# Kernel optimization log

Hardware: AMD Instinct MI355X
Metric: run time of the kernel (lower is better)

## Reference

```python
import jax, jax.numpy as jnp
import numpy as np

EPS = 1e-12  # torch F.normalize eps


def setup_inputs() -> dict:
    key = jax.random.key(0)
    k1, k2, k3, k4, k5 = jax.random.split(key, 5)
    N, C, H, W = 32, 512, 32, 32
    E = 1024   # expansion * dim
    G = 8      # group
    D = E // G # 128, per-group channel dim
    K = 64     # num_clusters
    x = jax.random.normal(k1, (N, C, H, W), dtype=jnp.float32)
    W1 = jax.random.normal(k2, (E, C), dtype=jnp.float32) / np.sqrt(C)
    W2 = jax.random.normal(k3, (G, E), dtype=jnp.float32) / np.sqrt(E)
    Wc = jax.random.normal(k4, (K, D), dtype=jnp.float32) / np.sqrt(D)
    centroids = jax.random.uniform(k5, (K, D), dtype=jnp.float32)
    return {"x": x, "W1": W1, "W2": W2, "Wc": Wc, "centroids": centroids}


def reference(x, W1, W2, Wc, centroids):
    # x: [N, C, H, W]; W1: [E, C]; W2: [G, E]; Wc: [K, D]; centroids: [K, D]
    N, C, H, W = x.shape
    E = W1.shape[0]
    G = W2.shape[0]
    K, D = Wc.shape
    P = H * W
    # descriptor-wise L2 normalization over channel dim
    norm = jnp.linalg.norm(x, axis=1, keepdims=True)
    x = x / jnp.maximum(norm, EPS)
    # linear1 on channels: [N, E, P]
    xe = jnp.einsum('ncp,ec->nep', x.reshape(N, C, P), W1)
    # grouped features: [N, G, D, P]
    xg = xe.reshape(N, G, D, P)
    # attention gate: sigmoid(linear2)  -> [N, G, P]
    att = jax.nn.sigmoid(jnp.einsum('nep,ge->ngp', xe, W2))
    # 1x1 conv = per-pixel matmul with cluster weights -> [N, G, K, P]
    soft_assign = jax.nn.softmax(jnp.einsum('ngdp,kd->ngkp', xg, Wc), axis=2)
    # combined per-(cluster,pixel) weight
    w = soft_assign * att[:, :, None, :]  # [N, G, K, P]
    # NetVLAD residual aggregation, algebraically decomposed to avoid the
    # giant [N,G,K,D,P] intermediate:
    #   vlad[n,k,d] = sum_{g,p} w * xg  -  centroids[k,d] * sum_{g,p} w
    agg = jnp.einsum('ngkp,ngdp->nkd', w, xg)  # [N, K, D]
    wsum = w.sum(axis=(1, 3))                  # [N, K]
    vlad = agg - wsum[:, :, None] * centroids[None]  # [N, K, D]
    return vlad.reshape(N, K * D)
```

## Files before the change

### kernel.cpp

```cpp
#include <hip/hip_runtime.h>


#define N_  32
#define C_  512
#define P_  1024
#define E_  1024
#define G_  8
#define D_  128
#define K_  64

typedef __attribute__((ext_vector_type(8))) short bf16x8;
typedef __attribute__((ext_vector_type(4))) float f32x4;

__device__ __forceinline__ unsigned short f2b(float f) {
    union { float f; unsigned u; } v; v.f = f;
    unsigned r = (v.u + 0x7FFFu + ((v.u >> 16) & 1u)) >> 16;
    return (unsigned short)r;
}
__device__ __forceinline__ float b2f(unsigned short h) {
    union { unsigned u; float f; } v; v.u = ((unsigned)h) << 16;
    return v.f;
}

__device__ __forceinline__ void gl_lds16(const void* g, void* l) {
    __builtin_amdgcn_global_load_lds(
        (const __attribute__((address_space(1))) void*)g,
        (__attribute__((address_space(3))) void*)l, 16, 0, 0);
}

__global__ __launch_bounds__(256) void k0_prep(const float* __restrict__ W1,
                                               const float* __restrict__ Wc,
                                               unsigned short* __restrict__ W1b,
                                               unsigned short* __restrict__ Vb) {
    int bid = blockIdx.x;
    int t = threadIdx.x;
    int i0 = bid * 512 + t;
    W1b[i0]       = f2b(W1[i0]);
    W1b[i0 + 256] = f2b(W1[i0 + 256]);
    int ch = bid & 1, k = (bid >> 1) & 63, g = bid >> 7;
    int c = ch * 256 + t;
    float acc = 0.f;
    #pragma unroll 8
    for (int d = 0; d < 128; ++d)
        acc += Wc[k * 128 + d] * W1[(g * 128 + d) * C_ + c];
    Vb[(g * 64 + k) * C_ + c] = f2b(acc);
}

__global__ __launch_bounds__(256) void k1_norm_transpose(const float* __restrict__ x,
                                                         unsigned short* __restrict__ xhat_t) {
    __shared__ short xc[128 * 256];
    __shared__ float red[256];
    __shared__ float rn[64];
    int n = blockIdx.y;
    int p0 = blockIdx.x * 64;
    int t = threadIdx.x;
    int ps = t & 63, cs = t >> 6;

    float ss = 0.f;
    for (int i = 0; i < 128; ++i) {
        float v = x[((size_t)(n * C_ + cs * 128 + i)) * P_ + p0 + ps];
        ss += v * v;
        xc[i * 256 + t] = (short)f2b(v);
    }
    red[t] = ss;
    __syncthreads();
    if (t < 64) {
        float s = red[t] + red[64 + t] + red[128 + t] + red[192 + t];
        rn[t] = 1.0f / fmaxf(sqrtf(s), 1e-12f);
    }
    __syncthreads();

    float r = rn[ps];
    size_t base = ((size_t)(n * P_ + p0 + ps)) * C_ + cs * 128;
    #pragma unroll
    for (int jj = 0; jj < 16; ++jj) {
        bf16x8 o;
        #pragma unroll
        for (int j = 0; j < 8; ++j)
            o[j] = (short)f2b(b2f((unsigned short)xc[(jj * 8 + j) * 256 + t]) * r);
        *(bf16x8*)&xhat_t[base + jj * 8] = o;
    }
}

__global__ __launch_bounds__(256) void k2_gemm_xe(const unsigned short* __restrict__ W1b,
                                                  const unsigned short* __restrict__ xhat_t,
                                                  const float* __restrict__ W2,
                                                  unsigned short* __restrict__ xe,
                                                  float* __restrict__ att_part) {
    __shared__ __align__(16) short As[128 * 64];
    __shared__ __align__(16) short Bs[128 * 64];
    int n = blockIdx.y;
    int e0 = (blockIdx.x >> 3) * 128;
    int p0 = (blockIdx.x & 7) * 128;
    int t = threadIdx.x;
    int w = t >> 6, l = t & 63, q = l >> 4, l15 = l & 15;
    int wr = w >> 1, wc = w & 1;

    f32x4 acc[4][4];
    #pragma unroll
    for (int mi = 0; mi < 4; ++mi)
        #pragma unroll
        for (int ni = 0; ni < 4; ++ni)
            acc[mi][ni] = (f32x4){0.f, 0.f, 0.f, 0.f};

    for (int ks = 0; ks < 8; ++ks) {
        int k0 = ks * 64;
        #pragma unroll
        for (int i = 0; i < 4; ++i) {
            int ch = i * 256 + t;
            int row = ch >> 3, col = (ch & 7) * 8;
            gl_lds16(&W1b[(e0 + row) * C_ + k0 + col], &As[ch * 8]);
        }
        #pragma unroll
        for (int i = 0; i < 4; ++i) {
            int ch = i * 256 + t;
            int row = ch >> 3, col = (ch & 7) * 8;
            gl_lds16(&xhat_t[((size_t)(n * P_ + p0 + row)) * C_ + k0 + col], &Bs[ch * 8]);
        }
        __syncthreads();

        #pragma unroll
        for (int kk = 0; kk < 2; ++kk) {
            bf16x8 af[4], bf[4];
            #pragma unroll
            for (int mi = 0; mi < 4; ++mi)
                af[mi] = *(const bf16x8*)&As[(wr * 64 + mi * 16 + l15) * 64 + kk * 32 + q * 8];
            #pragma unroll
            for (int ni = 0; ni < 4; ++ni)
                bf[ni] = *(const bf16x8*)&Bs[(wc * 64 + ni * 16 + l15) * 64 + kk * 32 + q * 8];
            #pragma unroll
            for (int mi = 0; mi < 4; ++mi)
                #pragma unroll
                for (int ni = 0; ni < 4; ++ni)
                    acc[mi][ni] = __builtin_amdgcn_mfma_f32_16x16x32_bf16(af[mi], bf[ni], acc[mi][ni], 0, 0, 0);
        }
        __syncthreads();
    }

    #pragma unroll
    for (int mi = 0; mi < 4; ++mi) {
        #pragma unroll
        for (int ni = 0; ni < 4; ++ni) {
            #pragma unroll
            for (int r = 0; r < 4; ++r) {
                int e = e0 + wr * 64 + mi * 16 + q * 4 + r;
                int p = p0 + wc * 64 + ni * 16 + l15;
                xe[((size_t)(n * E_ + e)) * P_ + p] = f2b(acc[mi][ni][r]);
            }
        }
    }

    float* w2l = (float*)As;
    #pragma unroll
    for (int i = 0; i < 4; ++i) {
        int idx = i * 256 + t;
        w2l[idx] = W2[(idx >> 7) * E_ + e0 + (idx & 127)];
    }
    __syncthreads();
    int slot = (blockIdx.x >> 3) * 2 + wr;
    #pragma unroll
    for (int gg = 0; gg < 8; ++gg) {
        float pa[4] = {0.f, 0.f, 0.f, 0.f};
        #pragma unroll
        for (int mi = 0; mi < 4; ++mi)
            #pragma unroll
            for (int r = 0; r < 4; ++r) {
                float w2v = w2l[gg * 128 + wr * 64 + mi * 16 + q * 4 + r];
                #pragma unroll
                for (int ni = 0; ni < 4; ++ni)
                    pa[ni] += acc[mi][ni][r] * w2v;
            }
        #pragma unroll
        for (int ni = 0; ni < 4; ++ni) {
            pa[ni] += __shfl_xor(pa[ni], 16);
            pa[ni] += __shfl_xor(pa[ni], 32);
        }
        if (q == 0) {
            size_t ab = (((size_t)(n * 16 + slot)) * 8 + gg) * P_ + p0 + wc * 64;
            #pragma unroll
            for (int ni = 0; ni < 4; ++ni)
                att_part[ab + ni * 16 + l15] = pa[ni];
        }
    }
}

__global__ __launch_bounds__(256) void k3b_att_reduce(const float* __restrict__ att_part,
                                                      float* __restrict__ att_s) {
    int idx = blockIdx.x * 256 + threadIdx.x;
    int p = idx & 1023;
    int g = (idx >> 10) & 7;
    int n = idx >> 13;
    float s = 0.f;
    #pragma unroll
    for (int sl = 0; sl < 16; ++sl)
        s += att_part[(((size_t)(n * 16 + sl)) * 8 + g) * P_ + p];
    att_s[idx] = 1.0f / (1.0f + __expf(-s));
}

__global__ __launch_bounds__(256) void k4_assign_agg(const unsigned short* __restrict__ Vb,
                                                     const unsigned short* __restrict__ xhat_t,
                                                     const unsigned short* __restrict__ xe,
                                                     const float* __restrict__ att_s,
                                                     float* __restrict__ agg_part,
                                                     float* __restrict__ wsum_part) {
    __shared__ __align__(16) char smem[18432 + 17408];
    short* As2   = (short*)smem;
    short* Bs2   = (short*)(smem + 4096);
    short* xglds = (short*)smem;
    short* wlds  = (short*)(smem + 18432);

    int bx = blockIdx.x;
    int qt = bx & 3, g = bx >> 2, n = blockIdx.y;
    int t = threadIdx.x;
    int w = t >> 6, l = t & 63, q = l >> 4, l15 = l & 15;

    f32x4 acc_a[4][2];
    #pragma unroll
    for (int mi = 0; mi < 4; ++mi)
        #pragma unroll
        for (int ni = 0; ni < 2; ++ni)
            acc_a[mi][ni] = (f32x4){0.f, 0.f, 0.f, 0.f};
    float wsp[16];
    #pragma unroll
    for (int j = 0; j < 16; ++j) wsp[j] = 0.f;

    for (int cc = 0; cc < 2; ++cc) {
        int p0c = qt * 256 + cc * 128;

        f32x4 acc_s[4][2];
        #pragma unroll
        for (int mi = 0; mi < 4; ++mi)
            #pragma unroll
            for (int ni = 0; ni < 2; ++ni)
                acc_s[mi][ni] = (f32x4){0.f, 0.f, 0.f, 0.f};

        for (int ks = 0; ks < 16; ++ks) {
            int k0 = ks * 32;
            {
                int row = t >> 2, col = (t & 3) * 8;
                gl_lds16(&Vb[(g * 64 + row) * C_ + k0 + col], &As2[t * 8]);
            }
            #pragma unroll
            for (int i = 0; i < 2; ++i) {
                int ch = i * 256 + t;
                int row = ch >> 2, col = (ch & 3) * 8;
                gl_lds16(&xhat_t[((size_t)(n * P_ + p0c + row)) * C_ + k0 + col], &Bs2[ch * 8]);
            }
            __syncthreads();
            bf16x8 af[4], bf2[2];
            #pragma unroll
            for (int mi = 0; mi < 4; ++mi)
                af[mi] = *(const bf16x8*)&As2[(mi * 16 + l15) * 32 + q * 8];
            #pragma unroll
            for (int ni = 0; ni < 2; ++ni)
                bf2[ni] = *(const bf16x8*)&Bs2[(w * 32 + ni * 16 + l15) * 32 + q * 8];
            #pragma unroll
            for (int mi = 0; mi < 4; ++mi)
                #pragma unroll
                for (int ni = 0; ni < 2; ++ni)
                    acc_s[mi][ni] = __builtin_amdgcn_mfma_f32_16x16x32_bf16(af[mi], bf2[ni], acc_s[mi][ni], 0, 0, 0);
            __syncthreads();
        }

        #pragma unroll
        for (int ni = 0; ni < 2; ++ni) {
            float m = -1e30f;
            #pragma unroll
            for (int mi = 0; mi < 4; ++mi)
                #pragma unroll
                for (int r = 0; r < 4; ++r)
                    m = fmaxf(m, acc_s[mi][ni][r]);
            m = fmaxf(m, __shfl_xor(m, 16));
            m = fmaxf(m, __shfl_xor(m, 32));
            float s = 0.f;
            #pragma unroll
            for (int mi = 0; mi < 4; ++mi)
                #pragma unroll
                for (int r = 0; r < 4; ++r) {
                    float e = __expf(acc_s[mi][ni][r] - m);
                    acc_s[mi][ni][r] = e;
                    s += e;
                }
            s += __shfl_xor(s, 16);
            s += __shfl_xor(s, 32);

            int pcol = p0c + w * 32 + ni * 16 + l15;
            float av = att_s[(((size_t)(n * G_ + g)) * P_) + pcol];
            float scale = av / s;

            #pragma unroll
            for (int mi = 0; mi < 4; ++mi)
                #pragma unroll
                for (int r = 0; r < 4; ++r) {
                    float wv = acc_s[mi][ni][r] * scale;
                    wsp[mi * 4 + r] += wv;
                    wlds[(mi * 16 + q * 4 + r) * 136 + (w * 32 + ni * 16 + l15)] = (short)f2b(wv);
                }
        }

        for (int h = 0; h < 2; ++h) {
            #pragma unroll
            for (int i = 0; i < 4; ++i) {
                int ch = i * 256 + t;
                int row = ch / 9, col = (ch % 9) * 8;
                gl_lds16(&xe[((size_t)(n * E_ + g * 128 + row)) * P_ + p0c + h * 64 + col],
                         &xglds[ch * 8]);
            }
            if (t < 128) {
                int ch = 1024 + t;
                int row = ch / 9, col = (ch % 9) * 8;
                gl_lds16(&xe[((size_t)(n * E_ + g * 128 + row)) * P_ + p0c + h * 64 + col],
                         &xglds[ch * 8]);
            }
            __syncthreads();

            #pragma unroll
            for (int pk = 0; pk < 2; ++pk) {
                bf16x8 a2[4], b2[2];
                #pragma unroll
                for (int mi = 0; mi < 4; ++mi)
                    a2[mi] = *(const bf16x8*)&wlds[(mi * 16 + l15) * 136 + h * 64 + pk * 32 + q * 8];
                #pragma unroll
                for (int ni = 0; ni < 2; ++ni)
                    b2[ni] = *(const bf16x8*)&xglds[(w * 32 + ni * 16 + l15) * 72 + pk * 32 + q * 8];
                #pragma unroll
                for (int mi = 0; mi < 4; ++mi)
                    #pragma unroll
                    for (int ni = 0; ni < 2; ++ni)
                        acc_a[mi][ni] = __builtin_amdgcn_mfma_f32_16x16x32_bf16(a2[mi], b2[ni], acc_a[mi][ni], 0, 0, 0);
            }
            __syncthreads();
        }
    }

    size_t base = (((size_t)(n * G_ + g)) * 4 + qt) * 64;
    #pragma unroll
    for (int mi = 0; mi < 4; ++mi)
        #pragma unroll
        for (int ni = 0; ni < 2; ++ni)
            #pragma unroll
            for (int r = 0; r < 4; ++r) {
                int k = mi * 16 + q * 4 + r;
                int d = w * 32 + ni * 16 + l15;
                agg_part[(base + k) * 128 + d] = acc_a[mi][ni][r];
            }

    #pragma unroll
    for (int j = 0; j < 16; ++j) {
        float v = wsp[j];
        v += __shfl_xor(v, 1);
        v += __shfl_xor(v, 2);
        v += __shfl_xor(v, 4);
        v += __shfl_xor(v, 8);
        if (l15 == 0) {
            int k = (j >> 2) * 16 + q * 4 + (j & 3);
            wsum_part[(base + 0) * 0 + ((((size_t)(n * G_ + g)) * 4 + qt) * 4 + w) * 64 + k] = v;
        }
    }
}

__global__ __launch_bounds__(256) void k4c_wsum(const float* __restrict__ wsum_part,
                                                float* __restrict__ wsum) {
    int idx = blockIdx.x * 256 + threadIdx.x;
    int n = idx >> 6, k = idx & 63;
    float s = 0.f;
    #pragma unroll
    for (int g = 0; g < 8; ++g)
        #pragma unroll
        for (int qt = 0; qt < 4; ++qt)
            #pragma unroll
            for (int w2 = 0; w2 < 4; ++w2)
                s += wsum_part[((((size_t)(n * G_ + g)) * 4 + qt) * 4 + w2) * 64 + k];
    wsum[idx] = s;
}

__global__ __launch_bounds__(256) void k5_final(const float* __restrict__ agg_part,
                                                const float* __restrict__ wsum,
                                                const float* __restrict__ centroids,
                                                float* __restrict__ out) {
    int idx = blockIdx.x * 256 + threadIdx.x;
    int d = idx & 127;
    int k = (idx >> 7) & 63;
    int n = idx >> 13;
    float ag = 0.f;
    #pragma unroll
    for (int g = 0; g < 8; ++g)
        #pragma unroll
        for (int qt = 0; qt < 4; ++qt)
            ag += agg_part[((((size_t)(n * G_ + g)) * 4 + qt) * 64 + k) * 128 + d];
    out[idx] = ag - wsum[n * 64 + k] * centroids[k * 128 + d];
}

extern "C" void kernel_launch(void* const* d_in, const int* in_sizes, int n_in,
                              void* d_out, int out_size, void* d_ws, size_t ws_size,
                              hipStream_t stream) {
    const float* x         = (const float*)d_in[0];
    const float* W1        = (const float*)d_in[1];
    const float* W2        = (const float*)d_in[2];
    const float* Wc        = (const float*)d_in[3];
    const float* centroids = (const float*)d_in[4];
    float* out = (float*)d_out;

    char* ws = (char*)d_ws;
    unsigned short* W1b      = (unsigned short*)(ws + 0);
    unsigned short* Vb       = (unsigned short*)(ws + 1048576);
    unsigned short* xhat_t   = (unsigned short*)(ws + 1572864);
    unsigned short* xe       = (unsigned short*)(ws + 35127296);
    float*          att_s    = (float*)(ws + 102236160);
    float*          att_part = (float*)(ws + 103284736);
    float*          agg_part = (float*)(ws + 103284736);
    float*          wsum_part= (float*)(ws + 136839168);
    float*          wsum     = (float*)(ws + 138936320);

    hipLaunchKernelGGL(k0_prep,        dim3(1024), dim3(256), 0, stream, W1, Wc, W1b, Vb);
    hipLaunchKernelGGL(k1_norm_transpose, dim3(16, 32), dim3(256), 0, stream, x, xhat_t);
    hipLaunchKernelGGL(k2_gemm_xe,     dim3(64, 32), dim3(256), 0, stream,
                       W1b, xhat_t, W2, xe, att_part);
    hipLaunchKernelGGL(k3b_att_reduce, dim3(1024), dim3(256), 0, stream, att_part, att_s);
    hipLaunchKernelGGL(k4_assign_agg,  dim3(32, 32), dim3(256), 0, stream, Vb, xhat_t, xe,
                       att_s, agg_part, wsum_part);
    hipLaunchKernelGGL(k4c_wsum,       dim3(8), dim3(256), 0, stream, wsum_part, wsum);
    hipLaunchKernelGGL(k5_final,       dim3(1024), dim3(256), 0, stream,
                       agg_part, wsum, centroids, out);
}
```

Measured before the change: 264.8 us.

## Fold cluster-score GEMM into main GEMM and precompute W2·W1 for attention

Stacks the precomputed Wc·W1 rows under W1 so a single GEMM launch produces both xe and the cluster scores S, removing the separate K=512 score GEMM inside the assign/aggregate kernel. Attention logits are now computed directly from normalized x using a precomputed W2·W1 matrix in a small kernel, replacing the partial-sum epilogue and its reduce kernel. Softmax is computed from S staged into LDS, and the weight sums are obtained with an extra MFMA against a ones vector. The cost is writing and re-reading the bf16 S tensor through global memory, a more serial per-column softmax over 128 threads, and bf16 rounding of the scores.

New measurement: 267.0 us. No clear change (+0.8%).

```diff
diff --git a/kernel.cpp b/kernel.cpp
--- a/kernel.cpp
+++ b/kernel.cpp
@@ -30,20 +30,36 @@
 
 __global__ __launch_bounds__(256) void k0_prep(const float* __restrict__ W1,
                                                const float* __restrict__ Wc,
-                                               unsigned short* __restrict__ W1b,
-                                               unsigned short* __restrict__ Vb) {
+                                               const float* __restrict__ W2,
+                                               unsigned short* __restrict__ AB,
+                                               float* __restrict__ W2W1) {
     int bid = blockIdx.x;
     int t = threadIdx.x;
-    int i0 = bid * 512 + t;
-    W1b[i0]       = f2b(W1[i0]);
-    W1b[i0 + 256] = f2b(W1[i0 + 256]);
-    int ch = bid & 1, k = (bid >> 1) & 63, g = bid >> 7;
-    int c = ch * 256 + t;
-    float acc = 0.f;
-    #pragma unroll 8
-    for (int d = 0; d < 128; ++d)
-        acc += Wc[k * 128 + d] * W1[(g * 128 + d) * C_ + c];
-    Vb[(g * 64 + k) * C_ + c] = f2b(acc);
+    if (bid < 1024) {
+        int i0 = bid * 512 + t;
+        AB[i0]       = f2b(W1[i0]);
+        AB[i0 + 256] = f2b(W1[i0 + 256]);
+        int ch = bid & 1, k = (bid >> 1) & 63, g = bid >> 7;
+        int c = ch * 256 + t;
+        float acc = 0.f;
+        #pragma unroll 8
+        for (int d = 0; d < 128; ++d)
+            acc += Wc[k * 128 + d] * W1[(g * 128 + d) * C_ + c];
+        AB[(1024 + g * 64 + k) * C_ + c] = f2b(acc);
+    } else {
+        int b2 = bid - 1024;
+        int out = b2 * 64 + (t >> 2);
+        int eq = t & 3;
+        int g = out >> 9, c = out & 511;
+        float acc = 0.f;
+        int e0 = eq * 256;
+        #pragma unroll 8
+        for (int e = e0; e < e0 + 256; ++e)
+            acc += W2[g * E_ + e] * W1[e * C_ + c];
+        acc += __shfl_xor(acc, 1);
+        acc += __shfl_xor(acc, 2);
+        if (eq == 0) W2W1[out] = acc;
+    }
 }
 
 __global__ __launch_bounds__(256) void k1_norm_transpose(const float* __restrict__ x,
@@ -82,11 +98,10 @@
     }
 }
 
-__global__ __launch_bounds__(256) void k2_gemm_xe(const unsigned short* __restrict__ W1b,
-                                                  const unsigned short* __restrict__ xhat_t,
-                                                  const float* __restrict__ W2,
-                                                  unsigned short* __restrict__ xe,
-                                                  float* __restrict__ att_part) {
+__global__ __launch_bounds__(256) void k2_gemm(const unsigned short* __restrict__ AB,
+                                               const unsigned short* __restrict__ xhat_t,
+                                               unsigned short* __restrict__ xe,
+                                               unsigned short* __restrict__ S) {
     __shared__ __align__(16) short As[128 * 64];
     __shared__ __align__(16) short Bs[128 * 64];
     int n = blockIdx.y;
@@ -109,7 +124,7 @@
         for (int i = 0; i < 4; ++i) {
             int ch = i * 256 + t;
             int row = ch >> 3, col = (ch & 7) * 8;
-            gl_lds16(&W1b[(e0 + row) * C_ + k0 + col], &As[ch * 8]);
+            gl_lds16(&AB[(e0 + row) * C_ + k0 + col], &As[ch * 8]);
         }
         #pragma unroll
         for (int i = 0; i < 4; ++i) {
@@ -137,166 +152,135 @@
         __syncthreads();
     }
 
-    #pragma unroll
-    for (int mi = 0; mi < 4; ++mi) {
-        #pragma unroll
-        for (int ni = 0; ni < 4; ++ni) {
-            #pragma unroll
-            for (int r = 0; r < 4; ++r) {
-                int e = e0 + wr * 64 + mi * 16 + q * 4 + r;
-                int p = p0 + wc * 64 + ni * 16 + l15;
-                xe[((size_t)(n * E_ + e)) * P_ + p] = f2b(acc[mi][ni][r]);
-            }
-        }
-    }
-
-    float* w2l = (float*)As;
-    #pragma unroll
-    for (int i = 0; i < 4; ++i) {
+    if (e0 < 1024) {
+        #pragma unroll
+        for (int mi = 0; mi < 4; ++mi)
+            #pragma unroll
+            for (int ni = 0; ni < 4; ++ni)
+                #pragma unroll
+                for (int r = 0; r < 4; ++r) {
+                    int e = e0 + wr * 64 + mi * 16 + q * 4 + r;
+                    int p = p0 + wc * 64 + ni * 16 + l15;
+                    xe[((size_t)(n * E_ + e)) * P_ + p] = f2b(acc[mi][ni][r]);
+                }
+    } else {
+        int s0 = e0 - 1024;
+        #pragma unroll
+        for (int mi = 0; mi < 4; ++mi)
+            #pragma unroll
+            for (int ni = 0; ni < 4; ++ni)
+                #pragma unroll
+                for (int r = 0; r < 4; ++r) {
+                    int sr = s0 + wr * 64 + mi * 16 + q * 4 + r;
+                    int p = p0 + wc * 64 + ni * 16 + l15;
+                    S[((size_t)(n * 512 + sr)) * P_ + p] = f2b(acc[mi][ni][r]);
+                }
+    }
+}
+
+__global__ __launch_bounds__(256) void k3_att(const unsigned short* __restrict__ xhat_t,
+                                              const float* __restrict__ W2W1,
+                                              float* __restrict__ att_s) {
+    __shared__ float w2l[512 * 8];
+    int n = blockIdx.y;
+    int t = threadIdx.x;
+    #pragma unroll
+    for (int i = 0; i < 16; ++i) {
         int idx = i * 256 + t;
-        w2l[idx] = W2[(idx >> 7) * E_ + e0 + (idx & 127)];
+        w2l[idx] = W2W1[(idx & 7) * C_ + (idx >> 3)];
     }
     __syncthreads();
-    int slot = (blockIdx.x >> 3) * 2 + wr;
-    #pragma unroll
-    for (int gg = 0; gg < 8; ++gg) {
-        float pa[4] = {0.f, 0.f, 0.f, 0.f};
-        #pragma unroll
-        for (int mi = 0; mi < 4; ++mi)
-            #pragma unroll
-            for (int r = 0; r < 4; ++r) {
-                float w2v = w2l[gg * 128 + wr * 64 + mi * 16 + q * 4 + r];
-                #pragma unroll
-                for (int ni = 0; ni < 4; ++ni)
-                    pa[ni] += acc[mi][ni][r] * w2v;
-            }
-        #pragma unroll
-        for (int ni = 0; ni < 4; ++ni) {
-            pa[ni] += __shfl_xor(pa[ni], 16);
-            pa[ni] += __shfl_xor(pa[ni], 32);
-        }
-        if (q == 0) {
-            size_t ab = (((size_t)(n * 16 + slot)) * 8 + gg) * P_ + p0 + wc * 64;
-            #pragma unroll
-            for (int ni = 0; ni < 4; ++ni)
-                att_part[ab + ni * 16 + l15] = pa[ni];
-        }
-    }
-}
-
-__global__ __launch_bounds__(256) void k3b_att_reduce(const float* __restrict__ att_part,
-                                                      float* __restrict__ att_s) {
-    int idx = blockIdx.x * 256 + threadIdx.x;
-    int p = idx & 1023;
-    int g = (idx >> 10) & 7;
-    int n = idx >> 13;
-    float s = 0.f;
-    #pragma unroll
-    for (int sl = 0; sl < 16; ++sl)
-        s += att_part[(((size_t)(n * 16 + sl)) * 8 + g) * P_ + p];
-    att_s[idx] = 1.0f / (1.0f + __expf(-s));
-}
-
-__global__ __launch_bounds__(256) void k4_assign_agg(const unsigned short* __restrict__ Vb,
-                                                     const unsigned short* __restrict__ xhat_t,
+
+    int px = blockIdx.x * 64 + (t >> 2);
+    int qc = t & 3;
+    const unsigned short* xrow = &xhat_t[((size_t)(n * P_ + px)) * C_ + qc * 128];
+    f32x4 a0 = {0.f, 0.f, 0.f, 0.f}, a1 = {0.f, 0.f, 0.f, 0.f};
+    #pragma unroll 4
+    for (int j = 0; j < 16; ++j) {
+        bf16x8 xv = *(const bf16x8*)&xrow[j * 8];
+        #pragma unroll
+        for (int ee = 0; ee < 8; ++ee) {
+            float v = b2f((unsigned short)xv[ee]);
+            int c = qc * 128 + j * 8 + ee;
+            a0 += v * *(const f32x4*)&w2l[c * 8];
+            a1 += v * *(const f32x4*)&w2l[c * 8 + 4];
+        }
+    }
+    #pragma unroll
+    for (int gg = 0; gg < 4; ++gg) {
+        a0[gg] += __shfl_xor(a0[gg], 1); a0[gg] += __shfl_xor(a0[gg], 2);
+        a1[gg] += __shfl_xor(a1[gg], 1); a1[gg] += __shfl_xor(a1[gg], 2);
+    }
+    if (qc == 0) {
+        #pragma unroll
+        for (int gg = 0; gg < 4; ++gg) {
+            att_s[((size_t)(n * G_ + gg)) * P_ + px]     = 1.0f / (1.0f + __expf(-a0[gg]));
+            att_s[((size_t)(n * G_ + gg + 4)) * P_ + px] = 1.0f / (1.0f + __expf(-a1[gg]));
+        }
+    }
+}
+
+__global__ __launch_bounds__(256) void k4_assign_agg(const unsigned short* __restrict__ S,
                                                      const unsigned short* __restrict__ xe,
                                                      const float* __restrict__ att_s,
                                                      float* __restrict__ agg_part,
                                                      float* __restrict__ wsum_part) {
     __shared__ __align__(16) char smem[18432 + 17408];
-    short* As2   = (short*)smem;
-    short* Bs2   = (short*)(smem + 4096);
+    short* slds  = (short*)smem;
     short* xglds = (short*)smem;
     short* wlds  = (short*)(smem + 18432);
 
-    int bx = blockIdx.x;
-    int qt = bx & 3, g = bx >> 2, n = blockIdx.y;
+    int qt = blockIdx.x & 3, g = blockIdx.x >> 2, n = blockIdx.y;
     int t = threadIdx.x;
     int w = t >> 6, l = t & 63, q = l >> 4, l15 = l & 15;
 
+    const short ONE = (short)0x3F80;
+    bf16x8 ones = {ONE, ONE, ONE, ONE, ONE, ONE, ONE, ONE};
+
     f32x4 acc_a[4][2];
     #pragma unroll
     for (int mi = 0; mi < 4; ++mi)
         #pragma unroll
         for (int ni = 0; ni < 2; ++ni)
             acc_a[mi][ni] = (f32x4){0.f, 0.f, 0.f, 0.f};
-    float wsp[16];
-    #pragma unroll
-    for (int j = 0; j < 16; ++j) wsp[j] = 0.f;
+    f32x4 acc_w[4];
+    #pragma unroll
+    for (int mi = 0; mi < 4; ++mi) acc_w[mi] = (f32x4){0.f, 0.f, 0.f, 0.f};
 
     for (int cc = 0; cc < 2; ++cc) {
         int p0c = qt * 256 + cc * 128;
 
-        f32x4 acc_s[4][2];
-        #pragma unroll
-        for (int mi = 0; mi < 4; ++mi)
-            #pragma unroll
-            for (int ni = 0; ni < 2; ++ni)
-                acc_s[mi][ni] = (f32x4){0.f, 0.f, 0.f, 0.f};
-
-        for (int ks = 0; ks < 16; ++ks) {
-            int k0 = ks * 32;
-            {
-                int row = t >> 2, col = (t & 3) * 8;
-                gl_lds16(&Vb[(g * 64 + row) * C_ + k0 + col], &As2[t * 8]);
+        #pragma unroll
+        for (int i = 0; i < 4; ++i) {
+            int ch = i * 256 + t;
+            int row = ch / 17, col = (ch % 17) * 8;
+            gl_lds16(&S[((size_t)(n * 512 + g * 64 + row)) * P_ + p0c + col], &slds[ch * 8]);
+        }
+        if (t < 64) {
+            int ch = 1024 + t;
+            int row = ch / 17, col = (ch % 17) * 8;
+            gl_lds16(&S[((size_t)(n * 512 + g * 64 + row)) * P_ + p0c + col], &slds[ch * 8]);
+        }
+        __syncthreads();
+
+        if (t < 128) {
+            float m = -1e30f;
+            #pragma unroll 8
+            for (int k = 0; k < 64; ++k)
+                m = fmaxf(m, b2f((unsigned short)slds[k * 136 + t]));
+            float s = 0.f;
+            float av = att_s[((size_t)(n * G_ + g)) * P_ + p0c + t];
+            #pragma unroll 8
+            for (int k = 0; k < 64; ++k)
+                s += __expf(b2f((unsigned short)slds[k * 136 + t]) - m);
+            float scale = av / s;
+            #pragma unroll 8
+            for (int k = 0; k < 64; ++k) {
+                float wv = __expf(b2f((unsigned short)slds[k * 136 + t]) - m) * scale;
+                wlds[k * 136 + t] = (short)f2b(wv);
             }
-            #pragma unroll
-            for (int i = 0; i < 2; ++i) {
-                int ch = i * 256 + t;
-                int row = ch >> 2, col = (ch & 3) * 8;
-                gl_lds16(&xhat_t[((size_t)(n * P_ + p0c + row)) * C_ + k0 + col], &Bs2[ch * 8]);
-            }
-            __syncthreads();
-            bf16x8 af[4], bf2[2];
-            #pragma unroll
-            for (int mi = 0; mi < 4; ++mi)
-                af[mi] = *(const bf16x8*)&As2[(mi * 16 + l15) * 32 + q * 8];
-            #pragma unroll
-            for (int ni = 0; ni < 2; ++ni)
-                bf2[ni] = *(const bf16x8*)&Bs2[(w * 32 + ni * 16 + l15) * 32 + q * 8];
-            #pragma unroll
-            for (int mi = 0; mi < 4; ++mi)
-                #pragma unroll
-                for (int ni = 0; ni < 2; ++ni)
-                    acc_s[mi][ni] = __builtin_amdgcn_mfma_f32_16x16x32_bf16(af[mi], bf2[ni], acc_s[mi][ni], 0, 0, 0);
-            __syncthreads();
-        }
-
-        #pragma unroll
-        for (int ni = 0; ni < 2; ++ni) {
-            float m = -1e30f;
-            #pragma unroll
-            for (int mi = 0; mi < 4; ++mi)
-                #pragma unroll
-                for (int r = 0; r < 4; ++r)
-                    m = fmaxf(m, acc_s[mi][ni][r]);
-            m = fmaxf(m, __shfl_xor(m, 16));
-            m = fmaxf(m, __shfl_xor(m, 32));
-            float s = 0.f;
-            #pragma unroll
-            for (int mi = 0; mi < 4; ++mi)
-                #pragma unroll
-                for (int r = 0; r < 4; ++r) {
-                    float e = __expf(acc_s[mi][ni][r] - m);
-                    acc_s[mi][ni][r] = e;
-                    s += e;
-                }
-            s += __shfl_xor(s, 16);
-            s += __shfl_xor(s, 32);
-
-            int pcol = p0c + w * 32 + ni * 16 + l15;
-            float av = att_s[(((size_t)(n * G_ + g)) * P_) + pcol];
-            float scale = av / s;
-
-            #pragma unroll
-            for (int mi = 0; mi < 4; ++mi)
-                #pragma unroll
-                for (int r = 0; r < 4; ++r) {
-                    float wv = acc_s[mi][ni][r] * scale;
-                    wsp[mi * 4 + r] += wv;
-                    wlds[(mi * 16 + q * 4 + r) * 136 + (w * 32 + ni * 16 + l15)] = (short)f2b(wv);
-                }
-        }
+        }
+        __syncthreads();
 
         for (int h = 0; h < 2; ++h) {
             #pragma unroll
@@ -324,10 +308,12 @@
                 for (int ni = 0; ni < 2; ++ni)
                     b2[ni] = *(const bf16x8*)&xglds[(w * 32 + ni * 16 + l15) * 72 + pk * 32 + q * 8];
                 #pragma unroll
-                for (int mi = 0; mi < 4; ++mi)
+                for (int mi = 0; mi < 4; ++mi) {
                     #pragma unroll
                     for (int ni = 0; ni < 2; ++ni)
                         acc_a[mi][ni] = __builtin_amdgcn_mfma_f32_16x16x32_bf16(a2[mi], b2[ni], acc_a[mi][ni], 0, 0, 0);
+                    acc_w[mi] = __builtin_amdgcn_mfma_f32_16x16x32_bf16(a2[mi], ones, acc_w[mi], 0, 0, 0);
+                }
             }
             __syncthreads();
         }
@@ -344,18 +330,12 @@
                 int d = w * 32 + ni * 16 + l15;
                 agg_part[(base + k) * 128 + d] = acc_a[mi][ni][r];
             }
-
-    #pragma unroll
-    for (int j = 0; j < 16; ++j) {
-        float v = wsp[j];
-        v += __shfl_xor(v, 1);
-        v += __shfl_xor(v, 2);
-        v += __shfl_xor(v, 4);
-        v += __shfl_xor(v, 8);
-        if (l15 == 0) {
-            int k = (j >> 2) * 16 + q * 4 + (j & 3);
-            wsum_part[(base + 0) * 0 + ((((size_t)(n * G_ + g)) * 4 + qt) * 4 + w) * 64 + k] = v;
-        }
+    if (w == 0 && l15 == 0) {
+        #pragma unroll
+        for (int mi = 0; mi < 4; ++mi)
+            #pragma unroll
+            for (int r = 0; r < 4; ++r)
+                wsum_part[base + mi * 16 + q * 4 + r] = acc_w[mi][r];
     }
 }
 
@@ -368,9 +348,7 @@
     for (int g = 0; g < 8; ++g)
         #pragma unroll
         for (int qt = 0; qt < 4; ++qt)
-            #pragma unroll
-            for (int w2 = 0; w2 < 4; ++w2)
-                s += wsum_part[((((size_t)(n * G_ + g)) * 4 + qt) * 4 + w2) * 64 + k];
+            s += wsum_part[(((size_t)(n * G_ + g)) * 4 + qt) * 64 + k];
     wsum[idx] = s;
 }
 
@@ -402,22 +380,21 @@
     float* out = (float*)d_out;
 
     char* ws = (char*)d_ws;
-    unsigned short* W1b      = (unsigned short*)(ws + 0);
-    unsigned short* Vb       = (unsigned short*)(ws + 1048576);
+    unsigned short* AB       = (unsigned short*)(ws + 0);
     unsigned short* xhat_t   = (unsigned short*)(ws + 1572864);
+    float*          agg_part = (float*)(ws + 1572864);
     unsigned short* xe       = (unsigned short*)(ws + 35127296);
     float*          att_s    = (float*)(ws + 102236160);
-    float*          att_part = (float*)(ws + 103284736);
-    float*          agg_part = (float*)(ws + 103284736);
+    unsigned short* S        = (unsigned short*)(ws + 103284736);
     float*          wsum_part= (float*)(ws + 136839168);
-    float*          wsum     = (float*)(ws + 138936320);
-
-    hipLaunchKernelGGL(k0_prep,        dim3(1024), dim3(256), 0, stream, W1, Wc, W1b, Vb);
+    float*          wsum     = (float*)(ws + 137363456);
+    float*          W2W1     = (float*)(ws + 137371648);
+
+    hipLaunchKernelGGL(k0_prep,        dim3(1088), dim3(256), 0, stream, W1, Wc, W2, AB, W2W1);
     hipLaunchKernelGGL(k1_norm_transpose, dim3(16, 32), dim3(256), 0, stream, x, xhat_t);
-    hipLaunchKernelGGL(k2_gemm_xe,     dim3(64, 32), dim3(256), 0, stream,
-                       W1b, xhat_t, W2, xe, att_part);
-    hipLaunchKernelGGL(k3b_att_reduce, dim3(1024), dim3(256), 0, stream, att_part, att_s);
-    hipLaunchKernelGGL(k4_assign_agg,  dim3(32, 32), dim3(256), 0, stream, Vb, xhat_t, xe,
+    hipLaunchKernelGGL(k2_gemm,        dim3(96, 32), dim3(256), 0, stream, AB, xhat_t, xe, S);
+    hipLaunchKernelGGL(k3_att,         dim3(16, 32), dim3(256), 0, stream, xhat_t, W2W1, att_s);
+    hipLaunchKernelGGL(k4_assign_agg,  dim3(32, 32), dim3(256), 0, stream, S, xe,
                        att_s, agg_part, wsum_part);
     hipLaunchKernelGGL(k4c_wsum,       dim3(8), dim3(256), 0, stream, wsum_part, wsum);
     hipLaunchKernelGGL(k5_final,       dim3(1024), dim3(256), 0, stream,
```
